# Optimization experiments

Hardware: AMD Instinct MI355X
Metric: run time of the kernel (lower is better)

## Reference

```python
import jax, jax.numpy as jnp
import numpy as np

N = 100000   # nodes
E = 600000   # edges
B = 512      # graphs in batch
H = 128      # hidden dim
ED = 8       # edge feature dim
TWO48 = float(2 ** 48 - 1)


def _w(k, shape, fan_in):
    return jax.random.normal(k, shape, jnp.float32) * (1.0 / np.sqrt(fan_in))


def setup_inputs() -> dict:
    key = jax.random.key(0)
    ks = jax.random.split(key, 32)
    inp = {}
    inp["s_node_ids"] = jax.random.randint(ks[0], (N,), 0, 2 ** 31 - 1, dtype=jnp.int32)
    inp["s_edge_index"] = jax.random.randint(ks[1], (2, E), 0, N, dtype=jnp.int32)
    inp["s_edge_attr"] = jax.random.normal(ks[2], (E, ED), jnp.float32)
    inp["s_batch"] = jnp.sort(jax.random.randint(ks[3], (N,), 0, B, dtype=jnp.int32))
    inp["depth"] = jax.random.uniform(ks[4], (B,), jnp.float32)
    # id_mlp: Linear(1,H) -> ReLU -> Linear(H,H)
    inp["id_w1"] = _w(ks[5], (1, H), 1); inp["id_b1"] = jnp.zeros((H,), jnp.float32)
    inp["id_w2"] = _w(ks[6], (H, H), H); inp["id_b2"] = jnp.zeros((H,), jnp.float32)
    # edge_mlp: Linear(ED,H) -> ReLU -> Linear(H,H)
    inp["ed_w1"] = _w(ks[7], (ED, H), ED); inp["ed_b1"] = jnp.zeros((H,), jnp.float32)
    inp["ed_w2"] = _w(ks[8], (H, H), H); inp["ed_b2"] = jnp.zeros((H,), jnp.float32)
    # GINEConv nn MLPs: Linear(H,H) -> ReLU -> Linear(H,H)
    inp["c1_w1"] = _w(ks[9], (H, H), H); inp["c1_b1"] = jnp.zeros((H,), jnp.float32)
    inp["c1_w2"] = _w(ks[10], (H, H), H); inp["c1_b2"] = jnp.zeros((H,), jnp.float32)
    inp["c2_w1"] = _w(ks[11], (H, H), H); inp["c2_b1"] = jnp.zeros((H,), jnp.float32)
    inp["c2_w2"] = _w(ks[12], (H, H), H); inp["c2_b2"] = jnp.zeros((H,), jnp.float32)
    inp["rg_w1"] = _w(ks[13], (H + 1, H), H + 1); inp["rg_b1"] = jnp.zeros((H,), jnp.float32)
    inp["rg_w2"] = _w(ks[14], (H, 1), H); inp["rg_b2"] = jnp.zeros((1,), jnp.float32)
    return inp


def _mlp2(x, w1, b1, w2, b2):
    return jax.nn.relu(x @ w1 + b1) @ w2 + b2


def _gine(x, src, dst, e, w1, b1, w2, b2):
    # message = ReLU(x_j + e), sum-aggregated at dst; out = nn((1+eps)*x + aggr), eps=0
    msg = jax.nn.relu(x[src] + e)                       # [E, H]
    aggr = jax.ops.segment_sum(msg, dst, num_segments=N)  # [N, H]
    return _mlp2(x + aggr, w1, b1, w2, b2)


def _global_mean(x, batch):
    sums = jax.ops.segment_sum(x, batch, num_segments=B)                          # [B, H]
    cnts = jax.ops.segment_sum(jnp.ones((x.shape[0], 1), x.dtype), batch, num_segments=B)
    return sums / jnp.maximum(cnts, 1.0)


def reference(s_node_ids, s_edge_index, s_edge_attr, s_batch, depth,
              id_w1, id_b1, id_w2, id_b2,
              ed_w1, ed_b1, ed_w2, ed_b2,
              c1_w1, c1_b1, c1_w2, c1_b2,
              c2_w1, c2_b1, c2_w2, c2_b2,
              rg_w1, rg_b1, rg_w2, rg_b2):
    src, dst = s_edge_index[0], s_edge_index[1]
    x0 = jnp.clip(s_node_ids.astype(jnp.float32) / TWO48, 0.0, 1.0)[:, None]  # [N,1]
    x = _mlp2(x0, id_w1, id_b1, id_w2, id_b2)                                 # [N,H]
    e = _mlp2(s_edge_attr, ed_w1, ed_b1, ed_w2, ed_b2)                        # [E,H]
    x = jax.nn.relu(_gine(x, src, dst, e, c1_w1, c1_b1, c1_w2, c1_b2))
    x = jax.nn.relu(_gine(x, src, dst, e, c2_w1, c2_b1, c2_w2, c2_b2))
    rep = jnp.concatenate([_global_mean(x, s_batch), depth[:, None]], axis=1)  # [B,H+1]
    return _mlp2(rep, rg_w1, rg_b1, rg_w2, rg_b2)[:, 0]                        # [B]
```

## Files before the change

kernel.cpp:

```cpp
#include <hip/hip_runtime.h>
#include <hip/hip_bf16.h>

#define N_NODES 100000
#define N_EDGES 600000
#define NB      512
#define H       128
#define ED      8
#define SCAN_CHUNK 1024
#define N_CHUNKS   98

typedef __attribute__((ext_vector_type(8))) short short8;
typedef __attribute__((ext_vector_type(4))) float f32x4;
typedef unsigned short u16;
typedef unsigned int   u32;

static __device__ __forceinline__ u16 f2bf(float f) {
    u32 u = __float_as_uint(f);
    u32 r = u + 0x7fffu + ((u >> 16) & 1u);
    return (u16)(r >> 16);
}
static __device__ __forceinline__ float bf2f(u32 h) {
    return __uint_as_float(h << 16);
}

__global__ __launch_bounds__(256) void pack_all_kernel(
    const float* __restrict__ W0, const float* __restrict__ W1,
    const float* __restrict__ W2, const float* __restrict__ W3,
    const float* __restrict__ W4, const float* __restrict__ W5,
    const float* __restrict__ W6,
    short8* __restrict__ O0, short8* __restrict__ O1,
    short8* __restrict__ O2, short8* __restrict__ O3,
    short8* __restrict__ O4, short8* __restrict__ O5,
    short8* __restrict__ O6)
{
    int gid = blockIdx.x * 256 + threadIdx.x;
    const int total = 512 + 6 * 2048;
    if (gid >= total) return;
    const float* W; short8* O; int Krows, kkmax, slot;
    if (gid < 512) { W = W0; O = O0; Krows = ED; kkmax = 1; slot = gid; }
    else {
        int m = (gid - 512) / 2048;
        slot = (gid - 512) % 2048;
        Krows = H; kkmax = 4;
        switch (m) {
            case 0: W = W1; O = O1; break;
            case 1: W = W2; O = O2; break;
            case 2: W = W3; O = O3; break;
            case 3: W = W4; O = O4; break;
            case 4: W = W5; O = O5; break;
            default: W = W6; O = O6; break;
        }
    }
    int lane = slot & 63;
    int t = slot >> 6;
    int nt = t & 1; t >>= 1;
    int kk = t % kkmax;
    int w  = t / kkmax;
    int quad = lane >> 4, n15 = lane & 15;
    int n = w * 32 + nt * 16 + n15;
    short8 v;
    #pragma unroll
    for (int j = 0; j < 8; j++) {
        int k = kk * 32 + quad * 8 + j;
        v[j] = (k < Krows) ? (short)f2bf(W[k * H + n]) : (short)0;
    }
    O[slot] = v;
}

__global__ __launch_bounds__(256) void hist_kernel(
    const int* __restrict__ edge_index, int* __restrict__ counts)
{
    int e = blockIdx.x * 256 + threadIdx.x;
    if (e < N_EDGES) atomicAdd(&counts[edge_index[N_EDGES + e]], 1);
}

__global__ __launch_bounds__(SCAN_CHUNK) void scan1_kernel(
    const int* __restrict__ counts, int* __restrict__ chunk_scan,
    int* __restrict__ bsum_raw)
{
    __shared__ int s[SCAN_CHUNK];
    int tid = threadIdx.x;
    int gid = blockIdx.x * SCAN_CHUNK + tid;
    int v = counts[gid];
    s[tid] = v;
    __syncthreads();
    #pragma unroll
    for (int off = 1; off < SCAN_CHUNK; off <<= 1) {
        int t = (tid >= off) ? s[tid - off] : 0;
        __syncthreads();
        s[tid] += t;
        __syncthreads();
    }
    chunk_scan[gid] = s[tid] - v;
    if (tid == SCAN_CHUNK - 1) bsum_raw[blockIdx.x] = s[tid];
}

__global__ __launch_bounds__(128) void scan2_kernel(
    const int* __restrict__ bsum_raw, int* __restrict__ bsum_scan)
{
    __shared__ int s[128];
    int tid = threadIdx.x;
    int v = (tid < N_CHUNKS) ? bsum_raw[tid] : 0;
    s[tid] = v;
    __syncthreads();
    #pragma unroll
    for (int off = 1; off < 128; off <<= 1) {
        int t = (tid >= off) ? s[tid - off] : 0;
        __syncthreads();
        s[tid] += t;
        __syncthreads();
    }
    bsum_scan[tid] = s[tid] - v;
}

__global__ __launch_bounds__(256) void fill_kernel(
    const int* __restrict__ edge_index,
    const int* __restrict__ chunk_scan, const int* __restrict__ bsum_scan,
    int* __restrict__ counts, int* __restrict__ src_list,
    int* __restrict__ pos_of)
{
    int e = blockIdx.x * 256 + threadIdx.x;
    if (e >= N_EDGES) return;
    int src = edge_index[e];
    int dst = edge_index[N_EDGES + e];
    int slot = atomicAdd(&counts[dst], -1) - 1;
    int pos = chunk_scan[dst] + bsum_scan[dst >> 10] + slot;
    src_list[pos] = src;
    pos_of[e] = pos;
}

__global__ __launch_bounds__(256) void finalize_offsets(
    const int* __restrict__ chunk_scan, const int* __restrict__ bsum_scan,
    int* __restrict__ row_start)
{
    int i = blockIdx.x * 256 + threadIdx.x;
    if (i <= N_NODES) row_start[i] = chunk_scan[i] + bsum_scan[i >> 10];
}

__global__ __launch_bounds__(256) void node_mlp_mfma(
    const int* __restrict__ ids,
    const float* __restrict__ w1, const float* __restrict__ b1,
    const short8* __restrict__ pW2, const float* __restrict__ b2,
    u16* __restrict__ x_out)
{
    __shared__ u16 sH[64 * 136];
    __shared__ float s_x0[64];
    int tid = threadIdx.x;
    int w = tid >> 6, lane = tid & 63, quad = lane >> 4, n15 = lane & 15;
    short8 fW2[4][2];
    #pragma unroll
    for (int kk = 0; kk < 4; kk++) {
        fW2[kk][0] = pW2[((w * 4 + kk) * 2 + 0) * 64 + lane];
        fW2[kk][1] = pW2[((w * 4 + kk) * 2 + 1) * 64 + lane];
    }
    float rb2[2] = { b2[w * 32 + n15], b2[w * 32 + 16 + n15] };
    float w1c = w1[tid & 127], b1c = b1[tid & 127];
    const int ntile = (N_NODES + 63) / 64;
    for (int tile = blockIdx.x; tile < ntile; tile += gridDim.x) {
        int row0 = tile * 64;
        if (tid < 64) {
            int n = row0 + tid;
            float x0 = (n < N_NODES) ? (float)ids[n] / 281474976710655.0f : 0.0f;
            s_x0[tid] = fminf(fmaxf(x0, 0.0f), 1.0f);
        }
        __syncthreads();
        int half = tid >> 7, c = tid & 127;
        #pragma unroll 8
        for (int rr = 0; rr < 32; rr++) {
            int r = half + rr * 2;
            sH[r * 136 + c] = f2bf(fmaxf(s_x0[r] * w1c + b1c, 0.0f));
        }
        __syncthreads();
        f32x4 acc[4][2];
        #pragma unroll
        for (int s = 0; s < 4; s++) { acc[s][0] = (f32x4){0,0,0,0}; acc[s][1] = (f32x4){0,0,0,0}; }
        #pragma unroll
        for (int kk = 0; kk < 4; kk++) {
            #pragma unroll
            for (int s = 0; s < 4; s++) {
                short8 a = *(const short8*)&sH[(s * 16 + n15) * 136 + kk * 32 + quad * 8];
                acc[s][0] = __builtin_amdgcn_mfma_f32_16x16x32_bf16(a, fW2[kk][0], acc[s][0], 0, 0, 0);
                acc[s][1] = __builtin_amdgcn_mfma_f32_16x16x32_bf16(a, fW2[kk][1], acc[s][1], 0, 0, 0);
            }
        }
        __syncthreads();
        #pragma unroll
        for (int s = 0; s < 4; s++)
            #pragma unroll
            for (int nt = 0; nt < 2; nt++) {
                int col = w * 32 + nt * 16 + n15;
                #pragma unroll
                for (int reg = 0; reg < 4; reg++)
                    sH[(s * 16 + quad * 4 + reg) * 136 + col] =
                        f2bf(acc[s][nt][reg] + rb2[nt]);
            }
        __syncthreads();
        for (int idx = tid; idx < 64 * 16; idx += 256) {
            int r = idx >> 4, c8 = (idx & 15) << 3;
            int n = row0 + r;
            if (n < N_NODES)
                *(uint4*)&x_out[(long)n * H + c8] = *(const uint4*)&sH[r * 136 + c8];
        }
        __syncthreads();
    }
}

__global__ __launch_bounds__(256) void edge_mlp_mfma(
    const float* __restrict__ attr,
    const int* __restrict__ pos_of,
    const short8* __restrict__ pW1, const float* __restrict__ b1,
    const short8* __restrict__ pW2, const float* __restrict__ b2,
    u16* __restrict__ e_perm)
{
    __shared__ u16 sA[64 * 40];
    __shared__ u16 sH[64 * 136];
    __shared__ int sPos[64];
    int tid = threadIdx.x;
    int w = tid >> 6, lane = tid & 63, quad = lane >> 4, n15 = lane & 15;
    short8 fW1[2];
    fW1[0] = pW1[(w * 2 + 0) * 64 + lane];
    fW1[1] = pW1[(w * 2 + 1) * 64 + lane];
    short8 fW2[4][2];
    #pragma unroll
    for (int kk = 0; kk < 4; kk++) {
        fW2[kk][0] = pW2[((w * 4 + kk) * 2 + 0) * 64 + lane];
        fW2[kk][1] = pW2[((w * 4 + kk) * 2 + 1) * 64 + lane];
    }
    float rb1[2] = { b1[w * 32 + n15], b1[w * 32 + 16 + n15] };
    float rb2[2] = { b2[w * 32 + n15], b2[w * 32 + 16 + n15] };
    const int ntile = N_EDGES / 64;
    for (int tile = blockIdx.x; tile < ntile; tile += gridDim.x) {
        int row0 = tile * 64;
        if (tid < 64) sPos[tid] = pos_of[row0 + tid];
        if (tid >= 64 && tid < 192) {
            int t2 = tid - 64;
            int r = t2 >> 1, c4 = (t2 & 1) * 4;
            float4 v = *(const float4*)&attr[(long)(row0 + r) * ED + c4];
            ushort4 o;
            o.x = f2bf(v.x); o.y = f2bf(v.y); o.z = f2bf(v.z); o.w = f2bf(v.w);
            *(ushort4*)&sA[r * 40 + c4] = o;
        } else if (tid >= 192) {
            int idx = tid - 192;
            for (; idx < 192; idx += 64) {
                int r = idx / 3, c8 = 8 + (idx % 3) * 8;
                *(uint4*)&sA[r * 40 + c8] = make_uint4(0, 0, 0, 0);
            }
        }
        __syncthreads();
        f32x4 acc[4][2];
        #pragma unroll
        for (int s = 0; s < 4; s++) { acc[s][0] = (f32x4){0,0,0,0}; acc[s][1] = (f32x4){0,0,0,0}; }
        #pragma unroll
        for (int s = 0; s < 4; s++) {
            short8 a = *(const short8*)&sA[(s * 16 + n15) * 40 + quad * 8];
            acc[s][0] = __builtin_amdgcn_mfma_f32_16x16x32_bf16(a, fW1[0], acc[s][0], 0, 0, 0);
            acc[s][1] = __builtin_amdgcn_mfma_f32_16x16x32_bf16(a, fW1[1], acc[s][1], 0, 0, 0);
        }
        #pragma unroll
        for (int s = 0; s < 4; s++)
            #pragma unroll
            for (int nt = 0; nt < 2; nt++) {
                int col = w * 32 + nt * 16 + n15;
                #pragma unroll
                for (int reg = 0; reg < 4; reg++)
                    sH[(s * 16 + quad * 4 + reg) * 136 + col] =
                        f2bf(fmaxf(acc[s][nt][reg] + rb1[nt], 0.0f));
            }
        __syncthreads();
        #pragma unroll
        for (int s = 0; s < 4; s++) { acc[s][0] = (f32x4){0,0,0,0}; acc[s][1] = (f32x4){0,0,0,0}; }
        #pragma unroll
        for (int kk = 0; kk < 4; kk++) {
            #pragma unroll
            for (int s = 0; s < 4; s++) {
                short8 a = *(const short8*)&sH[(s * 16 + n15) * 136 + kk * 32 + quad * 8];
                acc[s][0] = __builtin_amdgcn_mfma_f32_16x16x32_bf16(a, fW2[kk][0], acc[s][0], 0, 0, 0);
                acc[s][1] = __builtin_amdgcn_mfma_f32_16x16x32_bf16(a, fW2[kk][1], acc[s][1], 0, 0, 0);
            }
        }
        __syncthreads();
        #pragma unroll
        for (int s = 0; s < 4; s++)
            #pragma unroll
            for (int nt = 0; nt < 2; nt++) {
                int col = w * 32 + nt * 16 + n15;
                #pragma unroll
                for (int reg = 0; reg < 4; reg++)
                    sH[(s * 16 + quad * 4 + reg) * 136 + col] =
                        f2bf(acc[s][nt][reg] + rb2[nt]);
            }
        __syncthreads();
        for (int idx = tid; idx < 64 * 16; idx += 256) {
            int r = idx >> 4, c8 = (idx & 15) << 3;
            long rr = sPos[r];
            *(uint4*)&e_perm[rr * H + c8] = *(const uint4*)&sH[r * 136 + c8];
        }
        __syncthreads();
    }
}

__global__ __launch_bounds__(256) void aggregate_kernel(
    const int* __restrict__ row_start,
    const int* __restrict__ src_list,
    const u16* __restrict__ e_perm,
    const u16* __restrict__ x,
    u16* __restrict__ xs_out)
{
    int wave = threadIdx.x >> 6;
    int lane = threadIdx.x & 63;
    int fo = lane * 2;
    const u16* xb = x + fo;
    const int ngroups = N_NODES / 4;
    for (int g = blockIdx.x; g < ngroups; g += gridDim.x) {
        int n = g * 4 + wave;
        int beg = row_start[n];
        int end = row_start[n + 1];
        float a0 = 0.0f, a1 = 0.0f;
        float b0 = 0.0f, b1 = 0.0f;
        float c0 = 0.0f, c1 = 0.0f;
        float d0 = 0.0f, d1 = 0.0f;
        for (int j0 = beg; j0 < end; j0 += 64) {
            int m = min(64, end - j0);
            int sv = (lane < m) ? src_list[j0 + lane] : 0;
            const u16* ej = e_perm + (long)j0 * H + fo;
            int j = 0;
            for (; j + 4 <= m; j += 4) {
                int s0 = __shfl(sv, j);
                int s1 = __shfl(sv, j + 1);
                int s2 = __shfl(sv, j + 2);
                int s3 = __shfl(sv, j + 3);
                u32 xv0 = *(const u32*)(xb + (long)s0 * H);
                u32 ev0 = *(const u32*)(ej + (long)(j + 0) * H);
                u32 xv1 = *(const u32*)(xb + (long)s1 * H);
                u32 ev1 = *(const u32*)(ej + (long)(j + 1) * H);
                u32 xv2 = *(const u32*)(xb + (long)s2 * H);
                u32 ev2 = *(const u32*)(ej + (long)(j + 2) * H);
                u32 xv3 = *(const u32*)(xb + (long)s3 * H);
                u32 ev3 = *(const u32*)(ej + (long)(j + 3) * H);
                a0 += fmaxf(bf2f(xv0 & 0xffff) + bf2f(ev0 & 0xffff), 0.0f);
                a1 += fmaxf(bf2f(xv0 >> 16)    + bf2f(ev0 >> 16),    0.0f);
                b0 += fmaxf(bf2f(xv1 & 0xffff) + bf2f(ev1 & 0xffff), 0.0f);
                b1 += fmaxf(bf2f(xv1 >> 16)    + bf2f(ev1 >> 16),    0.0f);
                c0 += fmaxf(bf2f(xv2 & 0xffff) + bf2f(ev2 & 0xffff), 0.0f);
                c1 += fmaxf(bf2f(xv2 >> 16)    + bf2f(ev2 >> 16),    0.0f);
                d0 += fmaxf(bf2f(xv3 & 0xffff) + bf2f(ev3 & 0xffff), 0.0f);
                d1 += fmaxf(bf2f(xv3 >> 16)    + bf2f(ev3 >> 16),    0.0f);
            }
            for (; j < m; j++) {
                int s0 = __shfl(sv, j);
                u32 xv0 = *(const u32*)(xb + (long)s0 * H);
                u32 ev0 = *(const u32*)(ej + (long)j * H);
                a0 += fmaxf(bf2f(xv0 & 0xffff) + bf2f(ev0 & 0xffff), 0.0f);
                a1 += fmaxf(bf2f(xv0 >> 16)    + bf2f(ev0 >> 16),    0.0f);
            }
        }
        u32 xself = *(const u32*)(xb + (long)n * H);
        float o0 = bf2f(xself & 0xffff) + ((a0 + b0) + (c0 + d0));
        float o1 = bf2f(xself >> 16)    + ((a1 + b1) + (c1 + d1));
        *(u32*)&xs_out[(long)n * H + fo] = (u32)f2bf(o0) | ((u32)f2bf(o1) << 16);
    }
}

__global__ __launch_bounds__(256) void conv_mlp_mfma(
    const u16* __restrict__ xs,
    const short8* __restrict__ pW1, const float* __restrict__ b1,
    const short8* __restrict__ pW2, const float* __restrict__ b2,
    u16* __restrict__ x_out)
{
    __shared__ u16 sA[64 * 136];
    __shared__ u16 sH[64 * 136];
    int tid = threadIdx.x;
    int w = tid >> 6, lane = tid & 63, quad = lane >> 4, n15 = lane & 15;
    short8 fW1[4][2], fW2[4][2];
    #pragma unroll
    for (int kk = 0; kk < 4; kk++) {
        fW1[kk][0] = pW1[((w * 4 + kk) * 2 + 0) * 64 + lane];
        fW1[kk][1] = pW1[((w * 4 + kk) * 2 + 1) * 64 + lane];
        fW2[kk][0] = pW2[((w * 4 + kk) * 2 + 0) * 64 + lane];
        fW2[kk][1] = pW2[((w * 4 + kk) * 2 + 1) * 64 + lane];
    }
    float rb1[2] = { b1[w * 32 + n15], b1[w * 32 + 16 + n15] };
    float rb2[2] = { b2[w * 32 + n15], b2[w * 32 + 16 + n15] };
    const int ntile = (N_NODES + 63) / 64;
    for (int tile = blockIdx.x; tile < ntile; tile += gridDim.x) {
        int row0 = tile * 64;
        for (int idx = tid; idx < 64 * 16; idx += 256) {
            int r = idx >> 4, c8 = (idx & 15) << 3;
            int n = row0 + r;
            uint4 v = make_uint4(0, 0, 0, 0);
            if (n < N_NODES) v = *(const uint4*)&xs[(long)n * H + c8];
            *(uint4*)&sA[r * 136 + c8] = v;
        }
        __syncthreads();
        f32x4 acc[4][2];
        #pragma unroll
        for (int s = 0; s < 4; s++) { acc[s][0] = (f32x4){0,0,0,0}; acc[s][1] = (f32x4){0,0,0,0}; }
        #pragma unroll
        for (int kk = 0; kk < 4; kk++) {
            #pragma unroll
            for (int s = 0; s < 4; s++) {
                short8 a = *(const short8*)&sA[(s * 16 + n15) * 136 + kk * 32 + quad * 8];
                acc[s][0] = __builtin_amdgcn_mfma_f32_16x16x32_bf16(a, fW1[kk][0], acc[s][0], 0, 0, 0);
                acc[s][1] = __builtin_amdgcn_mfma_f32_16x16x32_bf16(a, fW1[kk][1], acc[s][1], 0, 0, 0);
            }
        }
        #pragma unroll
        for (int s = 0; s < 4; s++)
            #pragma unroll
            for (int nt = 0; nt < 2; nt++) {
                int col = w * 32 + nt * 16 + n15;
                #pragma unroll
                for (int reg = 0; reg < 4; reg++)
                    sH[(s * 16 + quad * 4 + reg) * 136 + col] =
                        f2bf(fmaxf(acc[s][nt][reg] + rb1[nt], 0.0f));
            }
        __syncthreads();
        #pragma unroll
        for (int s = 0; s < 4; s++) { acc[s][0] = (f32x4){0,0,0,0}; acc[s][1] = (f32x4){0,0,0,0}; }
        #pragma unroll
        for (int kk = 0; kk < 4; kk++) {
            #pragma unroll
            for (int s = 0; s < 4; s++) {
                short8 a = *(const short8*)&sH[(s * 16 + n15) * 136 + kk * 32 + quad * 8];
                acc[s][0] = __builtin_amdgcn_mfma_f32_16x16x32_bf16(a, fW2[kk][0], acc[s][0], 0, 0, 0);
                acc[s][1] = __builtin_amdgcn_mfma_f32_16x16x32_bf16(a, fW2[kk][1], acc[s][1], 0, 0, 0);
            }
        }
        #pragma unroll
        for (int s = 0; s < 4; s++)
            #pragma unroll
            for (int nt = 0; nt < 2; nt++) {
                int col = w * 32 + nt * 16 + n15;
                #pragma unroll
                for (int reg = 0; reg < 4; reg++)
                    sA[(s * 16 + quad * 4 + reg) * 136 + col] =
                        f2bf(fmaxf(acc[s][nt][reg] + rb2[nt], 0.0f));
            }
        __syncthreads();
        for (int idx = tid; idx < 64 * 16; idx += 256) {
            int r = idx >> 4, c8 = (idx & 15) << 3;
            int n = row0 + r;
            if (n < N_NODES)
                *(uint4*)&x_out[(long)n * H + c8] = *(const uint4*)&sA[r * 136 + c8];
        }
        __syncthreads();
    }
}

__global__ __launch_bounds__(256) void pool_kernel(
    const u16* __restrict__ x, const int* __restrict__ batch,
    float* __restrict__ sums, float* __restrict__ cnt)
{
    int sg   = threadIdx.x >> 6;
    int lane = threadIdx.x & 63;
    int fo = lane * 2;
    const int nper = (N_NODES + gridDim.x - 1) / gridDim.x;
    int n0 = blockIdx.x * nper;
    int n1 = min(n0 + nper, N_NODES);
    int cur = -1;
    float a0 = 0.0f, a1 = 0.0f, c = 0.0f;
    for (int n = n0 + sg; n < n1; n += 4) {
        int b = batch[n];
        if (b != cur) {
            if (cur >= 0) {
                atomicAdd(&sums[cur * H + fo],     a0);
                atomicAdd(&sums[cur * H + fo + 1], a1);
                if (lane == 0) atomicAdd(&cnt[cur], c);
            }
            a0 = a1 = 0.0f; c = 0.0f; cur = b;
        }
        u32 xv = *(const u32*)&x[(long)n * H + fo];
        a0 += bf2f(xv & 0xffff);
        a1 += bf2f(xv >> 16);
        c += 1.0f;
    }
    if (cur >= 0) {
        atomicAdd(&sums[cur * H + fo],     a0);
        atomicAdd(&sums[cur * H + fo + 1], a1);
        if (lane == 0) atomicAdd(&cnt[cur], c);
    }
}

__global__ __launch_bounds__(128) void regressor_kernel(
    const float* __restrict__ sums, const float* __restrict__ cnt,
    const float* __restrict__ depth,
    const float* __restrict__ w1, const float* __restrict__ b1,
    const float* __restrict__ w2, const float* __restrict__ b2,
    float* __restrict__ out)
{
    __shared__ float s_mean[H];
    __shared__ float s_red[2];
    int b = blockIdx.x;
    int j = threadIdx.x;
    float c = fmaxf(cnt[b], 1.0f);
    s_mean[j] = sums[b * H + j] / c;
    __syncthreads();
    float h = b1[j];
    #pragma unroll 8
    for (int k = 0; k < H; k++) h += s_mean[k] * w1[k * H + j];
    h += depth[b] * w1[H * H + j];
    h = fmaxf(h, 0.0f);
    float p = h * w2[j];
    #pragma unroll
    for (int off = 32; off >= 1; off >>= 1) p += __shfl_down(p, off, 64);
    if ((j & 63) == 0) s_red[j >> 6] = p;
    __syncthreads();
    if (j == 0) out[b] = s_red[0] + s_red[1] + b2[0];
}

extern "C" void kernel_launch(void* const* d_in, const int* in_sizes, int n_in,
                              void* d_out, int out_size, void* d_ws, size_t ws_size,
                              hipStream_t stream)
{
    const int*   ids   = (const int*)  d_in[0];
    const int*   eidx  = (const int*)  d_in[1];
    const float* eattr = (const float*)d_in[2];
    const int*   batch = (const int*)  d_in[3];
    const float* depth = (const float*)d_in[4];
    const float* id_w1 = (const float*)d_in[5];
    const float* id_b1 = (const float*)d_in[6];
    const float* id_w2 = (const float*)d_in[7];
    const float* id_b2 = (const float*)d_in[8];
    const float* ed_w1 = (const float*)d_in[9];
    const float* ed_b1 = (const float*)d_in[10];
    const float* ed_w2 = (const float*)d_in[11];
    const float* ed_b2 = (const float*)d_in[12];
    const float* c1_w1 = (const float*)d_in[13];
    const float* c1_b1 = (const float*)d_in[14];
    const float* c1_w2 = (const float*)d_in[15];
    const float* c1_b2 = (const float*)d_in[16];
    const float* c2_w1 = (const float*)d_in[17];
    const float* c2_b1 = (const float*)d_in[18];
    const float* c2_w2 = (const float*)d_in[19];
    const float* c2_b2 = (const float*)d_in[20];
    const float* rg_w1 = (const float*)d_in[21];
    const float* rg_b1 = (const float*)d_in[22];
    const float* rg_w2 = (const float*)d_in[23];
    const float* rg_b2 = (const float*)d_in[24];

    char* ws = (char*)d_ws;
    u16*   e_buf    = (u16*)  (ws);
    u16*   x_buf    = (u16*)  (ws + 153600000);
    u16*   xs_buf   = (u16*)  (ws + 179200000);
    float* sums_buf = (float*)(ws + 204800000);
    float* cnt_buf  = (float*)(ws + 205062144);
    int*   counts   = (int*)  (ws + 205064192);
    int*   chunk_sc = (int*)  (ws + 205465600);
    int*   bsum_raw = (int*)  (ws + 205867008);
    int*   bsum_sc  = (int*)  (ws + 205867520);
    int*   src_list = (int*)  (ws + 205868032);
    int*   pos_of   = (int*)  (ws + 208268032);
    short8* ed_w1p  = (short8*)(ws + 210668032);
    short8* ed_w2p  = (short8*)(ws + 210676224);
    short8* c1_w1p  = (short8*)(ws + 210708992);
    short8* c1_w2p  = (short8*)(ws + 210741760);
    short8* c2_w1p  = (short8*)(ws + 210774528);
    short8* c2_w2p  = (short8*)(ws + 210807296);
    short8* id_w2p  = (short8*)(ws + 210840064);
    int*   row_start = counts;

    pack_all_kernel<<<50, 256, 0, stream>>>(
        ed_w1, ed_w2, c1_w1, c1_w2, c2_w1, c2_w2, id_w2,
        ed_w1p, ed_w2p, c1_w1p, c1_w2p, c2_w1p, c2_w2p, id_w2p);

    hipMemsetAsync(counts, 0, 401408, stream);
    hist_kernel <<<(N_EDGES + 255) / 256, 256, 0, stream>>>(eidx, counts);
    scan1_kernel<<<N_CHUNKS, SCAN_CHUNK, 0, stream>>>(counts, chunk_sc, bsum_raw);
    scan2_kernel<<<1, 128, 0, stream>>>(bsum_raw, bsum_sc);
    fill_kernel <<<(N_EDGES + 255) / 256, 256, 0, stream>>>(eidx, chunk_sc, bsum_sc,
                                                            counts, src_list, pos_of);
    finalize_offsets<<<(N_NODES + 256) / 256, 256, 0, stream>>>(chunk_sc, bsum_sc, row_start);

    node_mlp_mfma<<<768, 256, 0, stream>>>(ids, id_w1, id_b1, id_w2p, id_b2, x_buf);
    edge_mlp_mfma<<<2048, 256, 0, stream>>>(eattr, pos_of, ed_w1p, ed_b1, ed_w2p, ed_b2, e_buf);

    aggregate_kernel<<<8192, 256, 0, stream>>>(row_start, src_list, e_buf, x_buf, xs_buf);
    conv_mlp_mfma<<<1563, 256, 0, stream>>>(xs_buf, c1_w1p, c1_b1, c1_w2p, c1_b2, x_buf);

    aggregate_kernel<<<8192, 256, 0, stream>>>(row_start, src_list, e_buf, x_buf, xs_buf);
    conv_mlp_mfma<<<1563, 256, 0, stream>>>(xs_buf, c2_w1p, c2_b1, c2_w2p, c2_b2, x_buf);

    hipMemsetAsync(sums_buf, 0, (size_t)(NB * H + NB) * 4, stream);
    pool_kernel<<<2048, 256, 0, stream>>>(x_buf, batch, sums_buf, cnt_buf);
    regressor_kernel<<<NB, 128, 0, stream>>>(sums_buf, cnt_buf, depth,
                                             rg_w1, rg_b1, rg_w2, rg_b2, (float*)d_out);
}
```

Before: 412.2 us.

## Aggregate with 16 lanes per node using 128-bit gathers

```diff
diff --git a/kernel.cpp b/kernel.cpp
--- a/kernel.cpp
+++ b/kernel.cpp
@@ -299,6 +299,16 @@
     }
 }
 
+static __device__ __forceinline__ void acc8(float* a, uint4 xv, uint4 ev) {
+    u32 xs[4] = { xv.x, xv.y, xv.z, xv.w };
+    u32 es[4] = { ev.x, ev.y, ev.z, ev.w };
+    #pragma unroll
+    for (int q = 0; q < 4; q++) {
+        a[2 * q + 0] += fmaxf(bf2f(xs[q] & 0xffff) + bf2f(es[q] & 0xffff), 0.0f);
+        a[2 * q + 1] += fmaxf(bf2f(xs[q] >> 16)    + bf2f(es[q] >> 16),    0.0f);
+    }
+}
+
 __global__ __launch_bounds__(256) void aggregate_kernel(
     const int* __restrict__ row_start,
     const int* __restrict__ src_list,
@@ -306,59 +316,54 @@
     const u16* __restrict__ x,
     u16* __restrict__ xs_out)
 {
-    int wave = threadIdx.x >> 6;
-    int lane = threadIdx.x & 63;
-    int fo = lane * 2;
+    int tid  = threadIdx.x;
+    int lane = tid & 63;
+    int l16  = lane & 15;
+    int base = lane & 48;
+    int fo   = l16 * 8;
+    int n = blockIdx.x * 16 + (tid >> 4);
     const u16* xb = x + fo;
-    const int ngroups = N_NODES / 4;
-    for (int g = blockIdx.x; g < ngroups; g += gridDim.x) {
-        int n = g * 4 + wave;
-        int beg = row_start[n];
-        int end = row_start[n + 1];
-        float a0 = 0.0f, a1 = 0.0f;
-        float b0 = 0.0f, b1 = 0.0f;
-        float c0 = 0.0f, c1 = 0.0f;
-        float d0 = 0.0f, d1 = 0.0f;
-        for (int j0 = beg; j0 < end; j0 += 64) {
-            int m = min(64, end - j0);
-            int sv = (lane < m) ? src_list[j0 + lane] : 0;
-            const u16* ej = e_perm + (long)j0 * H + fo;
-            int j = 0;
-            for (; j + 4 <= m; j += 4) {
-                int s0 = __shfl(sv, j);
-                int s1 = __shfl(sv, j + 1);
-                int s2 = __shfl(sv, j + 2);
-                int s3 = __shfl(sv, j + 3);
-                u32 xv0 = *(const u32*)(xb + (long)s0 * H);
-                u32 ev0 = *(const u32*)(ej + (long)(j + 0) * H);
-                u32 xv1 = *(const u32*)(xb + (long)s1 * H);
-                u32 ev1 = *(const u32*)(ej + (long)(j + 1) * H);
-                u32 xv2 = *(const u32*)(xb + (long)s2 * H);
-                u32 ev2 = *(const u32*)(ej + (long)(j + 2) * H);
-                u32 xv3 = *(const u32*)(xb + (long)s3 * H);
-                u32 ev3 = *(const u32*)(ej + (long)(j + 3) * H);
-                a0 += fmaxf(bf2f(xv0 & 0xffff) + bf2f(ev0 & 0xffff), 0.0f);
-                a1 += fmaxf(bf2f(xv0 >> 16)    + bf2f(ev0 >> 16),    0.0f);
-                b0 += fmaxf(bf2f(xv1 & 0xffff) + bf2f(ev1 & 0xffff), 0.0f);
-                b1 += fmaxf(bf2f(xv1 >> 16)    + bf2f(ev1 >> 16),    0.0f);
-                c0 += fmaxf(bf2f(xv2 & 0xffff) + bf2f(ev2 & 0xffff), 0.0f);
-                c1 += fmaxf(bf2f(xv2 >> 16)    + bf2f(ev2 >> 16),    0.0f);
-                d0 += fmaxf(bf2f(xv3 & 0xffff) + bf2f(ev3 & 0xffff), 0.0f);
-                d1 += fmaxf(bf2f(xv3 >> 16)    + bf2f(ev3 >> 16),    0.0f);
-            }
-            for (; j < m; j++) {
-                int s0 = __shfl(sv, j);
-                u32 xv0 = *(const u32*)(xb + (long)s0 * H);
-                u32 ev0 = *(const u32*)(ej + (long)j * H);
-                a0 += fmaxf(bf2f(xv0 & 0xffff) + bf2f(ev0 & 0xffff), 0.0f);
-                a1 += fmaxf(bf2f(xv0 >> 16)    + bf2f(ev0 >> 16),    0.0f);
-            }
-        }
-        u32 xself = *(const u32*)(xb + (long)n * H);
-        float o0 = bf2f(xself & 0xffff) + ((a0 + b0) + (c0 + d0));
-        float o1 = bf2f(xself >> 16)    + ((a1 + b1) + (c1 + d1));
-        *(u32*)&xs_out[(long)n * H + fo] = (u32)f2bf(o0) | ((u32)f2bf(o1) << 16);
-    }
+
+    int beg = row_start[n];
+    int end = row_start[n + 1];
+    float a[8], b[8];
+    #pragma unroll
+    for (int q = 0; q < 8; q++) { a[q] = 0.0f; b[q] = 0.0f; }
+
+    for (int j0 = beg; j0 < end; j0 += 16) {
+        int m = min(16, end - j0);
+        int sv = src_list[j0 + min(l16, m - 1)];
+        const u16* ej = e_perm + (long)j0 * H + fo;
+        int j = 0;
+        for (; j + 2 <= m; j += 2) {
+            int s0 = __shfl(sv, base | j);
+            int s1 = __shfl(sv, base | (j + 1));
+            uint4 xv0 = *(const uint4*)(xb + (long)s0 * H);
+            uint4 ev0 = *(const uint4*)(ej + (long)(j + 0) * H);
+            uint4 xv1 = *(const uint4*)(xb + (long)s1 * H);
+            uint4 ev1 = *(const uint4*)(ej + (long)(j + 1) * H);
+            acc8(a, xv0, ev0);
+            acc8(b, xv1, ev1);
+        }
+        if (j < m) {
+            int s0 = __shfl(sv, base | j);
+            uint4 xv0 = *(const uint4*)(xb + (long)s0 * H);
+            uint4 ev0 = *(const uint4*)(ej + (long)j * H);
+            acc8(a, xv0, ev0);
+        }
+    }
+    uint4 xself = *(const uint4*)(xb + (long)n * H);
+    u32 xs[4] = { xself.x, xself.y, xself.z, xself.w };
+    uint4 out;
+    u32 ov[4];
+    #pragma unroll
+    for (int q = 0; q < 4; q++) {
+        float o0 = bf2f(xs[q] & 0xffff) + a[2 * q + 0] + b[2 * q + 0];
+        float o1 = bf2f(xs[q] >> 16)    + a[2 * q + 1] + b[2 * q + 1];
+        ov[q] = (u32)f2bf(o0) | ((u32)f2bf(o1) << 16);
+    }
+    out.x = ov[0]; out.y = ov[1]; out.z = ov[2]; out.w = ov[3];
+    *(uint4*)&xs_out[(long)n * H + fo] = out;
 }
 
 __global__ __launch_bounds__(256) void conv_mlp_mfma(
@@ -574,10 +579,10 @@
     node_mlp_mfma<<<768, 256, 0, stream>>>(ids, id_w1, id_b1, id_w2p, id_b2, x_buf);
     edge_mlp_mfma<<<2048, 256, 0, stream>>>(eattr, pos_of, ed_w1p, ed_b1, ed_w2p, ed_b2, e_buf);
 
-    aggregate_kernel<<<8192, 256, 0, stream>>>(row_start, src_list, e_buf, x_buf, xs_buf);
+    aggregate_kernel<<<6250, 256, 0, stream>>>(row_start, src_list, e_buf, x_buf, xs_buf);
     conv_mlp_mfma<<<1563, 256, 0, stream>>>(xs_buf, c1_w1p, c1_b1, c1_w2p, c1_b2, x_buf);
 
-    aggregate_kernel<<<8192, 256, 0, stream>>>(row_start, src_list, e_buf, x_buf, xs_buf);
+    aggregate_kernel<<<6250, 256, 0, stream>>>(row_start, src_list, e_buf, x_buf, xs_buf);
     conv_mlp_mfma<<<1563, 256, 0, stream>>>(xs_buf, c2_w1p, c2_b1, c2_w2p, c2_b2, x_buf);
 
     hipMemsetAsync(sums_buf, 0, (size_t)(NB * H + NB) * 4, stream);
```

New measurement: 406.3 us. About the same (-1.4%).
